# Performance work log

Hardware: AMD Instinct MI355X
Metric: run time of the kernel (lower is better)

## Reference

```python
import jax, jax.numpy as jnp
import numpy as np


def setup_inputs() -> dict:
    key = jax.random.key(0)
    k1, k2 = jax.random.split(key)
    B, T, D = 16, 2048, 1024
    inputs = jax.random.normal(k1, (B, T, D), dtype=jnp.float32)
    mask = jax.random.randint(k2, (B, T), 0, 2).astype(bool)
    return {"inputs": inputs, "mask": mask}


def reference(inputs, mask):
    """Batched stream compaction (JIT-compatible ragged representation).

    Original TF layer loops over the batch and, per sample, gathers the
    rows of inputs[i] where mask[i] is True, returning ragged lists of
    (collected_values, valid_indices). Since JAX requires static shapes,
    we return the padded-compacted equivalent:
      collected: [B, T, D]  valid rows moved to the front (order preserved),
                            invalid tail zeroed.
      valid_idx: [B, T]     original timestep index of each collected row,
                            -1 in the padded tail.
      counts:    [B]        number of valid rows per sample, i.e.
                            collected[i, :counts[i]] == ragged segment i.
    """
    # Stable argsort of the inverted mask puts valid positions first,
    # preserving their original order -> single-pass prefix-sum compaction.
    order = jnp.argsort(jnp.logical_not(mask), axis=1, stable=True)      # [B, T]
    sorted_valid = jnp.take_along_axis(mask, order, axis=1)              # [B, T]
    collected = jnp.take_along_axis(inputs, order[:, :, None], axis=1)   # [B, T, D]
    collected = jnp.where(sorted_valid[:, :, None], collected, 0.0)
    valid_idx = jnp.where(sorted_valid, order, -1)
    counts = jnp.sum(mask, axis=1)
    return collected, valid_idx, counts
```

## Files before the change

kernel.cpp:

```cpp
#include <hip/hip_runtime.h>


#define BB 16
#define TT 2048
#define DD 1024

__global__ __launch_bounds__(256) void scan_kernel(
    const int* __restrict__ mask,
    float* __restrict__ out_vidx,
    float* __restrict__ out_counts,
    int* __restrict__ ws_src,
    int* __restrict__ ws_cnt)
{
    const int b = blockIdx.x;
    const int tid = threadIdx.x;
    const int* m = mask + b * TT;

    int vals[8];
    int s = 0;
#pragma unroll
    for (int i = 0; i < 8; ++i) {
        vals[i] = (m[tid * 8 + i] != 0) ? 1 : 0;
        s += vals[i];
    }

    __shared__ int sdata[256];
    sdata[tid] = s;
    __syncthreads();
#pragma unroll
    for (int off = 1; off < 256; off <<= 1) {
        int v = (tid >= off) ? sdata[tid - off] : 0;
        __syncthreads();
        sdata[tid] += v;
        __syncthreads();
    }
    const int excl = sdata[tid] - s;
    const int total = sdata[255];

    int pos = excl;
#pragma unroll
    for (int i = 0; i < 8; ++i) {
        if (vals[i]) {
            const int t = tid * 8 + i;
            ws_src[b * TT + pos] = t;
            out_vidx[b * TT + pos] = (float)t;
            ++pos;
        }
    }

    for (int c = total + tid; c < TT; c += 256) {
        out_vidx[b * TT + c] = -1.0f;
    }

    if (tid == 0) {
        ws_cnt[b] = total;
        out_counts[b] = (float)total;
    }
}

__global__ __launch_bounds__(256) void gather_kernel(
    const float* __restrict__ in,
    const int* __restrict__ ws_src,
    const int* __restrict__ ws_cnt,
    float* __restrict__ out)
{
    const int row = blockIdx.x;
    const int b = row >> 11;
    const int c = row & (TT - 1);
    const int tid = threadIdx.x;

    float4* dst = (float4*)(out + (size_t)row * DD);
    if (c < ws_cnt[b]) {
        const int src = ws_src[row];
        const float4* s = (const float4*)(in + ((size_t)b * TT + src) * DD);
        dst[tid] = s[tid];
    } else {
        dst[tid] = make_float4(0.f, 0.f, 0.f, 0.f);
    }
}

extern "C" void kernel_launch(void* const* d_in, const int* in_sizes, int n_in,
                              void* d_out, int out_size, void* d_ws, size_t ws_size,
                              hipStream_t stream) {
    const float* inputs = (const float*)d_in[0];
    const int* mask = (const int*)d_in[1];

    float* out = (float*)d_out;
    float* out_collected = out;
    float* out_vidx = out + (size_t)BB * TT * DD;
    float* out_counts = out_vidx + (size_t)BB * TT;

    int* ws_src = (int*)d_ws;
    int* ws_cnt = ws_src + BB * TT;

    scan_kernel<<<BB, 256, 0, stream>>>(mask, out_vidx, out_counts, ws_src, ws_cnt);
    gather_kernel<<<BB * TT, 256, 0, stream>>>(inputs, ws_src, ws_cnt, out_collected);
}
```

Measured before the change: 222.0 us.

## Gather 8 rows per block with nontemporal vector loads and stores

The gather kernel now has each 32-lane group copy one row, so a block of 256 threads handles 8 rows and the grid shrinks by 8x. Each lane issues 8 independent 16-byte loads before its stores, and all loads and stores use nontemporal builtins to bypass cache retention for the streamed data. The scan kernel also reads the mask with int4 loads. The aim is less per-block launch and scheduling overhead and more memory-level parallelism on a bandwidth-bound copy. The cost is higher register use per thread and fewer blocks in flight.

```diff
diff --git a/kernel.cpp b/kernel.cpp
--- a/kernel.cpp
+++ b/kernel.cpp
@@ -4,6 +4,9 @@
 #define BB 16
 #define TT 2048
 #define DD 1024
+#define ROW4 (DD / 4)
+
+typedef float f4 __attribute__((ext_vector_type(4)));
 
 __global__ __launch_bounds__(256) void scan_kernel(
     const int* __restrict__ mask,
@@ -14,15 +17,18 @@
 {
     const int b = blockIdx.x;
     const int tid = threadIdx.x;
-    const int* m = mask + b * TT;
+    const int4* m4 = (const int4*)(mask + b * TT);
 
+    int4 a0 = m4[tid * 2];
+    int4 a1 = m4[tid * 2 + 1];
     int vals[8];
+    vals[0] = (a0.x != 0); vals[1] = (a0.y != 0);
+    vals[2] = (a0.z != 0); vals[3] = (a0.w != 0);
+    vals[4] = (a1.x != 0); vals[5] = (a1.y != 0);
+    vals[6] = (a1.z != 0); vals[7] = (a1.w != 0);
     int s = 0;
 #pragma unroll
-    for (int i = 0; i < 8; ++i) {
-        vals[i] = (m[tid * 8 + i] != 0) ? 1 : 0;
-        s += vals[i];
-    }
+    for (int i = 0; i < 8; ++i) s += vals[i];
 
     __shared__ int sdata[256];
     sdata[tid] = s;
@@ -59,23 +65,34 @@
 }
 
 __global__ __launch_bounds__(256) void gather_kernel(
-    const float* __restrict__ in,
+    const f4* __restrict__ in,
     const int* __restrict__ ws_src,
     const int* __restrict__ ws_cnt,
-    float* __restrict__ out)
+    f4* __restrict__ out)
 {
-    const int row = blockIdx.x;
-    const int b = row >> 11;
-    const int c = row & (TT - 1);
-    const int tid = threadIdx.x;
+    const int tid  = threadIdx.x;
+    const int lrow = tid >> 5;
+    const int lane = tid & 31;
+    const int row  = blockIdx.x * 8 + lrow;
+    const int b    = row >> 11;
+    const int c    = row & (TT - 1);
 
-    float4* dst = (float4*)(out + (size_t)row * DD);
+    f4* dst = out + (size_t)row * ROW4;
     if (c < ws_cnt[b]) {
         const int src = ws_src[row];
-        const float4* s = (const float4*)(in + ((size_t)b * TT + src) * DD);
-        dst[tid] = s[tid];
+        const f4* sp = in + ((size_t)(b << 11) + (size_t)src) * ROW4;
+        f4 v[8];
+#pragma unroll
+        for (int j = 0; j < 8; ++j)
+            v[j] = __builtin_nontemporal_load(sp + lane + j * 32);
+#pragma unroll
+        for (int j = 0; j < 8; ++j)
+            __builtin_nontemporal_store(v[j], dst + lane + j * 32);
     } else {
-        dst[tid] = make_float4(0.f, 0.f, 0.f, 0.f);
+        const f4 z = {0.f, 0.f, 0.f, 0.f};
+#pragma unroll
+        for (int j = 0; j < 8; ++j)
+            __builtin_nontemporal_store(z, dst + lane + j * 32);
     }
 }
 
@@ -94,5 +111,6 @@
     int* ws_cnt = ws_src + BB * TT;
 
     scan_kernel<<<BB, 256, 0, stream>>>(mask, out_vidx, out_counts, ws_src, ws_cnt);
-    gather_kernel<<<BB * TT, 256, 0, stream>>>(inputs, ws_src, ws_cnt, out_collected);
+    gather_kernel<<<BB * TT / 8, 256, 0, stream>>>(
+        (const f4*)inputs, ws_src, ws_cnt, (f4*)out_collected);
 }
```

Result: no change. 218.0 us (-1.8%).
